# Kernel optimization log

Hardware: AMD Instinct MI355X
Metric: run time of the kernel (lower is better)

Reference implementation:

```python
import jax, jax.numpy as jnp
import numpy as np

HIDDEN = 1024
D_INNER = 2048
DT_RANK = 64
STATE = 16
KCONV = 4


def setup_inputs() -> dict:
    key = jax.random.key(0)
    ks = jax.random.split(key, 9)
    s = lambda k, shape, sc=0.02: jax.random.normal(k, shape, dtype=jnp.float32) * sc
    return {
        "x": jax.random.normal(ks[0], (2, 1024, HIDDEN), dtype=jnp.float32),
        "in_proj_w": s(ks[1], (2 * D_INNER, HIDDEN)),
        "conv_w": s(ks[2], (D_INNER, 1, KCONV), 0.2),
        "conv_b": s(ks[3], (D_INNER,), 0.1),
        "x_proj_w": s(ks[4], (DT_RANK + 2 * STATE, D_INNER)),
        "dt_proj_w": s(ks[5], (D_INNER, DT_RANK), 0.1),
        "dt_proj_b": s(ks[6], (D_INNER,), 0.1),
        "A_log": s(ks[7], (D_INNER, STATE), 0.5),
        "out_proj_w": s(ks[8], (HIDDEN, D_INNER)),
    }


def _selective_scan(u, delta, A, B, C):
    # u, delta: (b,l,d); A: (d,n); B, C: (b,l,n)
    deltaA = jnp.exp(delta[..., None] * A)               # (b,l,d,n)
    dBu = (delta * u)[..., None] * B[:, :, None, :]      # (b,l,d,n)
    # scan over time axis; carry h: (b,d,n)
    deltaA_t = jnp.moveaxis(deltaA, 1, 0)                # (l,b,d,n)
    dBu_t = jnp.moveaxis(dBu, 1, 0)                      # (l,b,d,n)
    C_t = jnp.moveaxis(C, 1, 0)                          # (l,b,n)

    def step(h, inp):
        dA_i, dBu_i, C_i = inp
        h = dA_i * h + dBu_i
        y = jnp.einsum('bdn,bn->bd', h, C_i)
        return h, y

    h0 = jnp.zeros(u.shape[:1] + u.shape[2:] + (A.shape[1],), dtype=u.dtype)
    _, ys = jax.lax.scan(step, h0, (deltaA_t, dBu_t, C_t))
    return jnp.moveaxis(ys, 0, 1)                        # (b,l,d)


def reference(x, in_proj_w, conv_w, conv_b, x_proj_w, dt_proj_w, dt_proj_b, A_log, out_proj_w):
    b, l, _ = x.shape
    xr = x @ in_proj_w.T                                 # (b,l,2*d_inner)
    xs, res = jnp.split(xr, 2, axis=-1)
    # causal depthwise conv1d: pad left k-1 (matches padding=k-1 then [:l])
    xc = jnp.moveaxis(xs, 1, 2)                          # (b,d,l)
    xc = jax.lax.conv_general_dilated(
        xc, conv_w, window_strides=(1,), padding=[(KCONV - 1, 0)],
        feature_group_count=D_INNER,
        dimension_numbers=('NCH', 'OIH', 'NCH'))
    xc = xc + conv_b[None, :, None]
    xs = jnp.moveaxis(xc, 2, 1)                          # (b,l,d)
    xs = jax.nn.silu(xs)
    x_dbl = xs @ x_proj_w.T                              # (b,l,dt_rank+2n)
    dt, B, C = jnp.split(x_dbl, [DT_RANK, DT_RANK + STATE], axis=-1)
    delta = jax.nn.softplus(dt @ dt_proj_w.T + dt_proj_b)
    A = -jnp.exp(A_log.astype(jnp.float32))
    y = _selective_scan(xs, delta, A, B, C)
    y = y * jax.nn.silu(res)
    return y @ out_proj_w.T
```

## Files before the change

### kernel.cpp

```cpp
#include <hip/hip_runtime.h>

typedef unsigned short u16;
typedef __bf16 bf16x8 __attribute__((ext_vector_type(8)));
typedef float f32x4 __attribute__((ext_vector_type(4)));

__device__ inline float bf2f(u16 u) {
    unsigned int x = ((unsigned int)u) << 16;
    return __builtin_bit_cast(float, x);
}
__device__ inline u16 f2bf(float f) {
    unsigned int x = __builtin_bit_cast(unsigned int, f);
    return (u16)((x + 0x7FFFu + ((x >> 16) & 1u)) >> 16);
}
__device__ inline float sigm(float v) { return 1.f / (1.f + __expf(-v)); }
__device__ inline float ex2(float x) {
    float r; asm("v_exp_f32 %0, %1" : "=v"(r) : "v"(x)); return r;
}

__device__ __forceinline__ void gload16(const void* g, void* l) {
    __builtin_amdgcn_global_load_lds(
        (const __attribute__((address_space(1))) void*)g,
        (__attribute__((address_space(3))) void*)l, 16, 0, 0);
}

__device__ inline uint4 pack8(const float* p) {
    const float4* q = (const float4*)p;
    float4 a = q[0], b = q[1];
    union { u16 h[8]; uint4 v; } u;
    u.h[0] = f2bf(a.x); u.h[1] = f2bf(a.y); u.h[2] = f2bf(a.z); u.h[3] = f2bf(a.w);
    u.h[4] = f2bf(b.x); u.h[5] = f2bf(b.y); u.h[6] = f2bf(b.z); u.h[7] = f2bf(b.w);
    return u.v;
}

__global__ __launch_bounds__(256)
void cvt_front(const float* __restrict__ x, const float* __restrict__ inw,
               const float* __restrict__ xpw, const float* __restrict__ convw,
               u16* __restrict__ x_bf, u16* __restrict__ inw_bf,
               u16* __restrict__ xpw_bf, float* __restrict__ wt)
{
    int bk = blockIdx.x, tid = threadIdx.x;
    if (bk < 1024) {
        int i = bk * 256 + tid;
        ((uint4*)x_bf)[i] = pack8(x + (size_t)i * 8);
    } else if (bk < 3072) {
        int i = (bk - 1024) * 256 + tid;
        ((uint4*)inw_bf)[i] = pack8(inw + (size_t)i * 8);
    } else if (bk < 3200) {
        int i = (bk - 3072) * 256 + tid;
        int row = (i * 8) >> 11;
        ((uint4*)xpw_bf)[i] = (row < 96) ? pack8(xpw + (size_t)row * 2048 + ((i * 8) & 2047))
                                         : make_uint4(0u, 0u, 0u, 0u);
    } else {
        int i = (bk - 3200) * 256 + tid;
        wt[(i & 3) * 2048 + (i >> 2)] = convw[i];
    }
}

template<int EPI, bool OUTF32, int BSRC>
__global__ __launch_bounds__(256, 2)
void gemm2(const u16* __restrict__ A, int lda,
           const void* __restrict__ Bv, int ldb,
           void* __restrict__ Cout, int ldc,
           int N, int ksplit, size_t zElems,
           const float* __restrict__ bias)
{
    __shared__ u16 sA[128][64];
    __shared__ u16 sB[128][64];

    const int tid  = threadIdx.x;
    const int lane = tid & 63;
    const int wave = tid >> 6;

    int nxy = gridDim.x * gridDim.y;
    int id  = blockIdx.y * gridDim.x + blockIdx.x;
    int bx, by;
    if ((nxy & 7) == 0) {
        int cpx = nxy >> 3;
        int swz = (id & 7) * cpx + (id >> 3);
        bx = swz % gridDim.x;
        by = swz / gridDim.x;
    } else { bx = blockIdx.x; by = blockIdx.y; }

    const int wm = (wave >> 1) * 64;
    const int wn = (wave & 1) * 64;
    const int m0 = by * 128;
    const int n0 = bx * 128;
    const int lm = lane & 15;
    const int g  = lane >> 4;
    const int k0 = blockIdx.z * ksplit;

    const int rr = lane >> 3;
    const int sl = lane & 7;
    const int xsl = sl ^ rr;
    const u16* gA = A + (size_t)(m0 + wave * 8 + rr) * lda + k0 + xsl * 8;
    const u16*  gB  = (BSRC == 0) ? (const u16*)Bv + (size_t)(n0 + wave * 8 + rr) * ldb + k0 + xsl * 8 : nullptr;
    const float* gBf = (BSRC == 1) ? (const float*)Bv + (size_t)(n0 + wave * 8 + rr) * ldb + k0 + xsl * 8 : nullptr;
    const int ldsRow = (wave * 8) * 128;

    f32x4 acc[4][4] = {};

    for (int kb = 0; kb < ksplit; kb += 64) {
        #pragma unroll
        for (int c = 0; c < 4; ++c) {
            gload16(gA + (size_t)c * 32 * lda + kb, (char*)sA + c * 4096 + ldsRow);
            if (BSRC == 0)
                gload16(gB + (size_t)c * 32 * ldb + kb, (char*)sB + c * 4096 + ldsRow);
        }
        if (BSRC == 1) {
            #pragma unroll
            for (int c = 0; c < 4; ++c) {
                uint4 v = pack8(gBf + (size_t)c * 32 * ldb + kb);
                *(uint4*)((char*)sB + c * 4096 + ldsRow + (lane << 4)) = v;
            }
        }
        __syncthreads();

        bf16x8 af[2][4], bfr[2][4];
        #pragma unroll
        for (int h = 0; h < 2; ++h) {
            #pragma unroll
            for (int i = 0; i < 4; ++i) {
                int ra = wm + i * 16 + lm;
                int rb = wn + i * 16 + lm;
                int chunk = (((h << 2) | g) ^ (lm & 7)) << 4;
                af[h][i]  = *(const bf16x8*)((const char*)sA + ra * 128 + chunk);
                bfr[h][i] = *(const bf16x8*)((const char*)sB + rb * 128 + chunk);
            }
        }
        #pragma unroll
        for (int h = 0; h < 2; ++h)
            #pragma unroll
            for (int i = 0; i < 4; ++i)
                #pragma unroll
                for (int j = 0; j < 4; ++j)
                    acc[i][j] = __builtin_amdgcn_mfma_f32_16x16x32_bf16(af[h][i], bfr[h][j], acc[i][j], 0, 0, 0);
        __syncthreads();
    }

    #pragma unroll
    for (int i = 0; i < 4; ++i) {
        int crow = m0 + wm + i * 16 + ((lane >> 4) << 2);
        #pragma unroll
        for (int j = 0; j < 4; ++j) {
            int ccol = n0 + wn + j * 16 + lm;
            if (ccol < N) {
                #pragma unroll
                for (int r = 0; r < 4; ++r) {
                    float v = acc[i][j][r];
                    if (EPI == 2 && ccol >= 2048) v *= sigm(v);
                    size_t off = (size_t)blockIdx.z * zElems + (size_t)(crow + r) * ldc + ccol;
                    if (OUTF32) ((float*)Cout)[off] = v;
                    else        ((u16*)Cout)[off]   = f2bf(v);
                }
            }
        }
    }
}

__global__ __launch_bounds__(256)
void dt_delta(const u16* __restrict__ xdbl, const float* __restrict__ dtw,
              const float* __restrict__ bias, u16* __restrict__ out)
{
    const int tid = threadIdx.x;
    const int d   = blockIdx.x * 256 + tid;
    const int t0  = blockIdx.y * 16;

    __shared__ float s_x[16][64];

    if (tid < 128) {
        int tok = tid >> 3, ch = tid & 7;
        uint4 v = *(const uint4*)&xdbl[(size_t)(t0 + tok) * 96 + ch * 8];
        const u16* h = (const u16*)&v;
        #pragma unroll
        for (int e = 0; e < 8; ++e) s_x[tok][ch * 8 + e] = bf2f(h[e]);
    }

    float w[64];
    {
        const float4* wp = (const float4*)(dtw + (size_t)d * 64);
        #pragma unroll
        for (int q = 0; q < 16; ++q) {
            float4 v = wp[q];
            w[q * 4 + 0] = v.x; w[q * 4 + 1] = v.y;
            w[q * 4 + 2] = v.z; w[q * 4 + 3] = v.w;
        }
    }
    const float bd = bias[d];
    __syncthreads();

    for (int tok = 0; tok < 16; ++tok) {
        float a0 = bd, a1 = 0.f, a2 = 0.f, a3 = 0.f;
        const float4* xv4 = (const float4*)s_x[tok];
        #pragma unroll
        for (int q = 0; q < 16; ++q) {
            float4 xv = xv4[q];
            a0 = fmaf(w[q * 4 + 0], xv.x, a0);
            a1 = fmaf(w[q * 4 + 1], xv.y, a1);
            a2 = fmaf(w[q * 4 + 2], xv.z, a2);
            a3 = fmaf(w[q * 4 + 3], xv.w, a3);
        }
        float v = (a0 + a1) + (a2 + a3);
        v = (v > 20.f) ? v : log1pf(__expf(v));
        out[(size_t)(t0 + tok) * 4096 + d] = f2bf(v);
    }
}

__global__ __launch_bounds__(256)
void reduce96(const float* __restrict__ splits, u16* __restrict__ xdbl)
{
    int i = blockIdx.x * 256 + threadIdx.x;
    float acc = 0.f;
    #pragma unroll
    for (int z = 0; z < 8; ++z) acc += splits[(size_t)z * 196608 + i];
    xdbl[i] = f2bf(acc);
}

__global__ __launch_bounds__(256)
void reduce_out(const u16* __restrict__ parts, float* __restrict__ out)
{
    int i = blockIdx.x * 256 + threadIdx.x;
    float acc[8] = {};
    #pragma unroll
    for (int z = 0; z < 4; ++z) {
        uint4 v = ((const uint4*)(parts + (size_t)z * 2097152))[i];
        const u16* h = (const u16*)&v;
        #pragma unroll
        for (int e = 0; e < 8; ++e) acc[e] += bf2f(h[e]);
    }
    float4* o = (float4*)(out + (size_t)i * 8);
    o[0] = make_float4(acc[0], acc[1], acc[2], acc[3]);
    o[1] = make_float4(acc[4], acc[5], acc[6], acc[7]);
}

__global__ __launch_bounds__(256)
void conv_silu(const u16* __restrict__ xr, const float* __restrict__ wt,
               const float* __restrict__ bias, u16* __restrict__ xs)
{
    int gi = blockIdx.x * 256 + threadIdx.x;
    int d  = (gi & 255) * 8;
    int t  = (gi >> 8) & 1023;
    int b  = gi >> 18;
    const u16* base = xr + (size_t)b * 4194304 + d;
    float acc[8];
    {
        const float4* bp = (const float4*)(bias + d);
        float4 b0 = bp[0], b1 = bp[1];
        acc[0]=b0.x; acc[1]=b0.y; acc[2]=b0.z; acc[3]=b0.w;
        acc[4]=b1.x; acc[5]=b1.y; acc[6]=b1.z; acc[7]=b1.w;
    }
    #pragma unroll
    for (int j = 0; j < 4; ++j) {
        int ti = t - 3 + j;
        if (ti >= 0) {
            uint4 v = *(const uint4*)(base + (size_t)ti * 4096);
            const u16* h = (const u16*)&v;
            const float4* wp = (const float4*)(wt + j * 2048 + d);
            float4 w0 = wp[0], w1 = wp[1];
            float w8[8] = {w0.x, w0.y, w0.z, w0.w, w1.x, w1.y, w1.z, w1.w};
            #pragma unroll
            for (int e = 0; e < 8; ++e) acc[e] = fmaf(w8[e], bf2f(h[e]), acc[e]);
        }
    }
    union { u16 h[8]; uint4 v; } o;
    #pragma unroll
    for (int e = 0; e < 8; ++e) { float v = acc[e]; o.h[e] = f2bf(v * sigm(v)); }
    ((uint4*)xs)[gi] = o.v;
}

template<int PHC>
__global__ __launch_bounds__(256)
void scan_chunk(const u16* __restrict__ deltag, u16* __restrict__ xsg,
                const u16* __restrict__ xdbl, const float* __restrict__ A_log,
                const u16* __restrict__ xr, float* __restrict__ summ,
                float* __restrict__ ssum)
{
    const int tid = threadIdx.x;
    const int d0 = blockIdx.x * 256;
    const int c  = blockIdx.y;
    const int b  = blockIdx.z;
    const int d  = d0 + tid;
    const int tok0 = b * 1024 + c * 32;

    __shared__ u16 s_del[32][256];
    __shared__ u16 s_uu[32][256];
    __shared__ u16 s_bc[32][32];
    __shared__ u16 s_res[PHC ? 32 : 1][PHC ? 256 : 1];
    __shared__ u16 s_y[PHC ? 32 : 1][PHC ? 256 : 1];

    for (int i = tid; i < 1024; i += 256) {
        int tl = i >> 5, v = i & 31;
        size_t tok = (size_t)(tok0 + tl);
        *(uint4*)&s_del[tl][v * 8] = *(const uint4*)&deltag[tok * 4096 + d0 + v * 8];
        *(uint4*)&s_uu[tl][v * 8]  = *(const uint4*)&xsg[tok * 2048 + d0 + v * 8];
        if (PHC)
            *(uint4*)&s_res[tl][v * 8] = *(const uint4*)&xr[tok * 4096 + 2048 + d0 + v * 8];
    }
    for (int i = tid; i < 1024; i += 256) {
        int tl = i >> 5, j = i & 31;
        s_bc[tl][j] = xdbl[(size_t)(tok0 + tl) * 96 + 64 + j];
    }

    float Ar[16], h[16];
    {
        const float4* Ap = (const float4*)(A_log + (size_t)d * 16);
        #pragma unroll
        for (int q = 0; q < 4; ++q) {
            float4 a = Ap[q];
            Ar[q * 4 + 0] = -__expf(a.x) * 1.44269504f;
            Ar[q * 4 + 1] = -__expf(a.y) * 1.44269504f;
            Ar[q * 4 + 2] = -__expf(a.z) * 1.44269504f;
            Ar[q * 4 + 3] = -__expf(a.w) * 1.44269504f;
        }
    }
    if (PHC) {
        const float4* hp = (const float4*)&summ[((size_t)(b * 32 + c) * 2048 + d) * 16];
        #pragma unroll
        for (int q = 0; q < 4; ++q) {
            float4 v = hp[q];
            h[q * 4 + 0] = v.x; h[q * 4 + 1] = v.y; h[q * 4 + 2] = v.z; h[q * 4 + 3] = v.w;
        }
    } else {
        #pragma unroll
        for (int n = 0; n < 16; ++n) h[n] = 0.f;
    }
    __syncthreads();

    float S = 0.f;
    #pragma unroll 4
    for (int tl = 0; tl < 32; ++tl) {
        float dlt = bf2f(s_del[tl][tid]);
        float du = dlt * bf2f(s_uu[tl][tid]);
        if (!PHC) S += dlt;
        #pragma unroll
        for (int n = 0; n < 16; ++n)
            h[n] = fmaf(ex2(dlt * Ar[n]), h[n], du * bf2f(s_bc[tl][n]));
        if (PHC) {
            float y = 0.f;
            #pragma unroll
            for (int n = 0; n < 16; ++n)
                y = fmaf(h[n], bf2f(s_bc[tl][16 + n]), y);
            s_y[tl][tid] = f2bf(y * bf2f(s_res[tl][tid]));
        }
    }

    if (!PHC) {
        float4* bp = (float4*)&summ[((size_t)(b * 32 + c) * 2048 + d) * 16];
        #pragma unroll
        for (int q = 0; q < 4; ++q)
            bp[q] = make_float4(h[q * 4], h[q * 4 + 1], h[q * 4 + 2], h[q * 4 + 3]);
        ssum[(size_t)(b * 32 + c) * 2048 + d] = S;
    } else {
        __syncthreads();
        for (int i = tid; i < 1024; i += 256) {
            int tl = i >> 5, v = i & 31;
            *(uint4*)&xsg[(size_t)(tok0 + tl) * 2048 + d0 + v * 8] = *(uint4*)&s_y[tl][v * 8];
        }
    }
}

__global__ __launch_bounds__(256)
void scan_phaseB(float* __restrict__ summ, const float* __restrict__ ssum,
                 const float* __restrict__ A_log)
{
    int g = blockIdx.x * 256 + threadIdx.x;
    int n = g & 15;
    int d = (g >> 4) & 2047;
    int b = g >> 15;
    float An2 = -__expf(A_log[(size_t)d * 16 + n]) * 1.44269504f;
    size_t base = ((size_t)(b * 32) * 2048 + d) * 16 + n;
    float bc[32], Sc[32];
    #pragma unroll
    for (int c = 0; c < 32; ++c) bc[c] = summ[base + (size_t)c * 32768];
    #pragma unroll
    for (int c = 0; c < 32; ++c) Sc[c] = ssum[(size_t)(b * 32 + c) * 2048 + d];
    float h = 0.f;
    #pragma unroll
    for (int c = 0; c < 32; ++c) {
        float nb = bc[c];
        bc[c] = h;
        h = fmaf(ex2(An2 * Sc[c]), h, nb);
    }
    #pragma unroll
    for (int c = 0; c < 32; ++c) summ[base + (size_t)c * 32768] = bc[c];
}

__global__ void sentinel_kernel(float* out, float v) { out[0] = v; }

extern "C" void kernel_launch(void* const* d_in, const int* in_sizes, int n_in,
                              void* d_out, int out_size, void* d_ws, size_t ws_size,
                              hipStream_t stream)
{
    const float* x         = (const float*)d_in[0];
    const float* in_w      = (const float*)d_in[1];
    const float* conv_w    = (const float*)d_in[2];
    const float* conv_b    = (const float*)d_in[3];
    const float* xproj_w   = (const float*)d_in[4];
    const float* dtproj_w  = (const float*)d_in[5];
    const float* dtproj_b  = (const float*)d_in[6];
    const float* A_log     = (const float*)d_in[7];
    const float* outproj_w = (const float*)d_in[8];
    float* out = (float*)d_out;

    static const int EXP[9] = {2097152, 4194304, 8192, 2048, 196608, 131072, 2048, 32768, 2097152};
    int bad = -1;
    if (n_in != 9) bad = 9;
    else { for (int i = 0; i < 9; ++i) if (in_sizes[i] != EXP[i]) { bad = i; break; } }
    if (bad < 0 && out_size != 2097152) bad = 10;
    if (bad < 0 && ws_size < 34734080u) bad = 11;
    if (bad >= 0) {
        sentinel_kernel<<<1, 1, 0, stream>>>(out, 131072.f * (1.f + (float)bad / 16.f));
        return;
    }

    char* ws = (char*)d_ws;
    u16*   xr      = (u16*)(ws);
    u16*   xs      = (u16*)(ws + 16777216);
    u16*   xdbl    = (u16*)(ws + 25165824);
    char*  R       = ws + 25559040;
    u16*   x_bf    = xs;
    u16*   inw_bf  = (u16*)(R);
    u16*   xpw_bf  = (u16*)(R + 8388608);
    float* wt      = (float*)(R + 8912896);
    float* splits  = (float*)(R);
    float* summ    = (float*)(R);
    float* ssum    = (float*)(R + 8388608);
    u16*   oparts  = xr;

    cvt_front<<<3232, 256, 0, stream>>>(x, in_w, xproj_w, conv_w,
                                        x_bf, inw_bf, xpw_bf, wt);
    gemm2<2, false, 0><<<dim3(32, 16, 1), 256, 0, stream>>>(
        x_bf, 1024, inw_bf, 1024, xr, 4096, 4096, 1024, 0, nullptr);
    conv_silu<<<2048, 256, 0, stream>>>(xr, wt, conv_b, xs);
    gemm2<0, true, 0><<<dim3(1, 16, 8), 256, 0, stream>>>(
        xs, 2048, xpw_bf, 2048, splits, 96, 96, 256, 196608, nullptr);
    reduce96<<<768, 256, 0, stream>>>(splits, xdbl);
    dt_delta<<<dim3(8, 128), 256, 0, stream>>>(xdbl, dtproj_w, dtproj_b, xr);
    scan_chunk<0><<<dim3(8, 32, 2), 256, 0, stream>>>(xr, xs, xdbl, A_log, xr, summ, ssum);
    scan_phaseB<<<256, 256, 0, stream>>>(summ, ssum, A_log);
    scan_chunk<1><<<dim3(8, 32, 2), 256, 0, stream>>>(xr, xs, xdbl, A_log, xr, summ, ssum);
    gemm2<0, false, 1><<<dim3(8, 16, 4), 256, 0, stream>>>(
        xs, 2048, outproj_w, 2048, oparts, 1024, 1024, 512, 2097152, nullptr);
    reduce_out<<<1024, 256, 0, stream>>>(oparts, out);
}
```

Baseline: 250.8 us.

## Pre-convert out_proj weights to bf16 and restructure dt_delta to token-parallel accumulation

A separate cvt_bf16 kernel now converts the out_proj weights to bf16 before the final GEMM. That GEMM can then load B through the async global-to-LDS path instead of converting fp32 in registers inside the tile loop, which also lets the BSRC template parameter go. dt_delta drops its shared-memory staging and 64-register weight array. It now streams weights one float4 at a time, keeps 16 per-token accumulators, and reads bf16 xdbl straight from global memory, relying on cache broadcast. The cost is one extra kernel launch plus an extra write and read of the weight matrix, and repeated global reads of xdbl in dt_delta.

```diff
diff --git a/kernel.cpp b/kernel.cpp
--- a/kernel.cpp
+++ b/kernel.cpp
@@ -56,10 +56,17 @@
     }
 }
 
-template<int EPI, bool OUTF32, int BSRC>
+__global__ __launch_bounds__(256)
+void cvt_bf16(const float* __restrict__ in, u16* __restrict__ out)
+{
+    int i = blockIdx.x * 256 + threadIdx.x;
+    ((uint4*)out)[i] = pack8(in + (size_t)i * 8);
+}
+
+template<int EPI, bool OUTF32>
 __global__ __launch_bounds__(256, 2)
 void gemm2(const u16* __restrict__ A, int lda,
-           const void* __restrict__ Bv, int ldb,
+           const u16* __restrict__ B, int ldb,
            void* __restrict__ Cout, int ldc,
            int N, int ksplit, size_t zElems,
            const float* __restrict__ bias)
@@ -93,8 +100,7 @@
     const int sl = lane & 7;
     const int xsl = sl ^ rr;
     const u16* gA = A + (size_t)(m0 + wave * 8 + rr) * lda + k0 + xsl * 8;
-    const u16*  gB  = (BSRC == 0) ? (const u16*)Bv + (size_t)(n0 + wave * 8 + rr) * ldb + k0 + xsl * 8 : nullptr;
-    const float* gBf = (BSRC == 1) ? (const float*)Bv + (size_t)(n0 + wave * 8 + rr) * ldb + k0 + xsl * 8 : nullptr;
+    const u16* gB = B + (size_t)(n0 + wave * 8 + rr) * ldb + k0 + xsl * 8;
     const int ldsRow = (wave * 8) * 128;
 
     f32x4 acc[4][4] = {};
@@ -103,15 +109,7 @@
         #pragma unroll
         for (int c = 0; c < 4; ++c) {
             gload16(gA + (size_t)c * 32 * lda + kb, (char*)sA + c * 4096 + ldsRow);
-            if (BSRC == 0)
-                gload16(gB + (size_t)c * 32 * ldb + kb, (char*)sB + c * 4096 + ldsRow);
-        }
-        if (BSRC == 1) {
-            #pragma unroll
-            for (int c = 0; c < 4; ++c) {
-                uint4 v = pack8(gBf + (size_t)c * 32 * ldb + kb);
-                *(uint4*)((char*)sB + c * 4096 + ldsRow + (lane << 4)) = v;
-            }
+            gload16(gB + (size_t)c * 32 * ldb + kb, (char*)sB + c * 4096 + ldsRow);
         }
         __syncthreads();
 
@@ -165,43 +163,33 @@
     const int d   = blockIdx.x * 256 + tid;
     const int t0  = blockIdx.y * 16;
 
-    __shared__ float s_x[16][64];
-
-    if (tid < 128) {
-        int tok = tid >> 3, ch = tid & 7;
-        uint4 v = *(const uint4*)&xdbl[(size_t)(t0 + tok) * 96 + ch * 8];
-        const u16* h = (const u16*)&v;
-        #pragma unroll
-        for (int e = 0; e < 8; ++e) s_x[tok][ch * 8 + e] = bf2f(h[e]);
-    }
-
-    float w[64];
-    {
-        const float4* wp = (const float4*)(dtw + (size_t)d * 64);
-        #pragma unroll
-        for (int q = 0; q < 16; ++q) {
-            float4 v = wp[q];
-            w[q * 4 + 0] = v.x; w[q * 4 + 1] = v.y;
-            w[q * 4 + 2] = v.z; w[q * 4 + 3] = v.w;
-        }
-    }
+    const float4* wp = (const float4*)(dtw + (size_t)d * 64);
     const float bd = bias[d];
-    __syncthreads();
-
-    for (int tok = 0; tok < 16; ++tok) {
-        float a0 = bd, a1 = 0.f, a2 = 0.f, a3 = 0.f;
-        const float4* xv4 = (const float4*)s_x[tok];
-        #pragma unroll
-        for (int q = 0; q < 16; ++q) {
-            float4 xv = xv4[q];
-            a0 = fmaf(w[q * 4 + 0], xv.x, a0);
-            a1 = fmaf(w[q * 4 + 1], xv.y, a1);
-            a2 = fmaf(w[q * 4 + 2], xv.z, a2);
-            a3 = fmaf(w[q * 4 + 3], xv.w, a3);
-        }
-        float v = (a0 + a1) + (a2 + a3);
+
+    float at[16];
+    #pragma unroll
+    for (int t = 0; t < 16; ++t) at[t] = bd;
+
+    float4 wq = wp[0];
+    #pragma unroll
+    for (int q = 0; q < 16; ++q) {
+        float4 wc = wq;
+        if (q < 15) wq = wp[q + 1];
+        #pragma unroll
+        for (int t = 0; t < 16; ++t) {
+            uint2 xv = *(const uint2*)(xdbl + (size_t)(t0 + t) * 96 + q * 4);
+            float x0 = __builtin_bit_cast(float, xv.x << 16);
+            float x1 = __builtin_bit_cast(float, xv.x & 0xFFFF0000u);
+            float x2 = __builtin_bit_cast(float, xv.y << 16);
+            float x3 = __builtin_bit_cast(float, xv.y & 0xFFFF0000u);
+            at[t] = fmaf(wc.x, x0, fmaf(wc.y, x1, fmaf(wc.z, x2, fmaf(wc.w, x3, at[t]))));
+        }
+    }
+    #pragma unroll
+    for (int t = 0; t < 16; ++t) {
+        float v = at[t];
         v = (v > 20.f) ? v : log1pf(__expf(v));
-        out[(size_t)(t0 + tok) * 4096 + d] = f2bf(v);
+        out[(size_t)(t0 + t) * 4096 + d] = f2bf(v);
     }
 }
 
@@ -424,21 +412,23 @@
     float* splits  = (float*)(R);
     float* summ    = (float*)(R);
     float* ssum    = (float*)(R + 8388608);
+    u16*   opw_bf  = (u16*)(R);
     u16*   oparts  = xr;
 
     cvt_front<<<3232, 256, 0, stream>>>(x, in_w, xproj_w, conv_w,
                                         x_bf, inw_bf, xpw_bf, wt);
-    gemm2<2, false, 0><<<dim3(32, 16, 1), 256, 0, stream>>>(
+    gemm2<2, false><<<dim3(32, 16, 1), 256, 0, stream>>>(
         x_bf, 1024, inw_bf, 1024, xr, 4096, 4096, 1024, 0, nullptr);
     conv_silu<<<2048, 256, 0, stream>>>(xr, wt, conv_b, xs);
-    gemm2<0, true, 0><<<dim3(1, 16, 8), 256, 0, stream>>>(
+    gemm2<0, true><<<dim3(1, 16, 8), 256, 0, stream>>>(
         xs, 2048, xpw_bf, 2048, splits, 96, 96, 256, 196608, nullptr);
     reduce96<<<768, 256, 0, stream>>>(splits, xdbl);
     dt_delta<<<dim3(8, 128), 256, 0, stream>>>(xdbl, dtproj_w, dtproj_b, xr);
     scan_chunk<0><<<dim3(8, 32, 2), 256, 0, stream>>>(xr, xs, xdbl, A_log, xr, summ, ssum);
     scan_phaseB<<<256, 256, 0, stream>>>(summ, ssum, A_log);
     scan_chunk<1><<<dim3(8, 32, 2), 256, 0, stream>>>(xr, xs, xdbl, A_log, xr, summ, ssum);
-    gemm2<0, false, 1><<<dim3(8, 16, 4), 256, 0, stream>>>(
-        xs, 2048, outproj_w, 2048, oparts, 1024, 1024, 512, 2097152, nullptr);
+    cvt_bf16<<<1024, 256, 0, stream>>>(outproj_w, opw_bf);
+    gemm2<0, false><<<dim3(8, 16, 4), 256, 0, stream>>>(
+        xs, 2048, opw_bf, 2048, oparts, 1024, 1024, 512, 2097152, nullptr);
     reduce_out<<<1024, 256, 0, stream>>>(oparts, out);
 }
```

Result: faster. 245.2 us (-2.2%).
